# Optimization experiments

Hardware: AMD Instinct MI355X
Metric: run time of the kernel (lower is better)

The kernel has to match this reference:

```python
import jax, jax.numpy as jnp
import numpy as np

N = 100000          # nodes
E = 1600000         # edges
F_IN = 32           # NUM_NODE_FEATURES
H = 128             # dim_h
G = 2048            # graphs in batch


def setup_inputs() -> dict:
    key = jax.random.key(0)
    ks = jax.random.split(key, 12)
    x = jax.random.normal(ks[0], (N, F_IN), dtype=jnp.float32)
    edge_index = jax.random.randint(ks[1], (2, E), 0, N, dtype=jnp.int64)
    batch = jnp.sort(jax.random.randint(ks[2], (N,), 0, G, dtype=jnp.int64))

    def glorot(k, fan_in, fan_out):
        s = np.sqrt(6.0 / (fan_in + fan_out)).astype(np.float32)
        return jax.random.uniform(k, (fan_in, fan_out), jnp.float32, -s, s)

    return {
        "x": x,
        "W1": glorot(ks[3], F_IN, H), "b1": jnp.zeros((H,), jnp.float32),
        "W2": glorot(ks[4], H, H),    "b2": jnp.zeros((H,), jnp.float32),
        "W3": glorot(ks[5], H, H),    "b3": jnp.zeros((H,), jnp.float32),
        "Wlin": glorot(ks[6], H, 1),  "blin": jnp.zeros((1,), jnp.float32),
        "edge_index": edge_index,
        "batch": batch,
    }


def _gcn_conv(x, W, b, row, col, norm, deg_inv):
    # PyG GCNConv: x' = D^{-1/2} (A + I) D^{-1/2} (x W) + b
    xw = x @ W                                   # [N, H]
    msg = norm[:, None] * xw[row]                # gather sources, scale per edge
    out = jax.ops.segment_sum(msg, col, num_segments=N)  # scatter-add to targets
    out = out + deg_inv[:, None] * xw            # self-loop term (norm = 1/deg)
    return out + b


def reference(x, W1, b1, W2, b2, W3, b3, Wlin, blin, edge_index, batch):
    row, col = edge_index[0], edge_index[1]      # source -> target
    # degrees including self-loops
    deg = jax.ops.segment_sum(jnp.ones((E,), x.dtype), col, num_segments=N) + 1.0
    d_isqrt = jax.lax.rsqrt(deg)
    norm = d_isqrt[row] * d_isqrt[col]           # per-edge symmetric norm
    deg_inv = d_isqrt * d_isqrt                  # self-loop norm = 1/deg

    h = jax.nn.relu(_gcn_conv(x, W1, b1, row, col, norm, deg_inv))
    h = jax.nn.relu(_gcn_conv(h, W2, b2, row, col, norm, deg_inv))
    h = _gcn_conv(h, W3, b3, row, col, norm, deg_inv)

    # global mean pool over graphs
    sums = jax.ops.segment_sum(h, batch, num_segments=G)           # [G, H]
    counts = jax.ops.segment_sum(jnp.ones((N,), h.dtype), batch, num_segments=G)
    pooled = sums / jnp.maximum(counts, 1.0)[:, None]

    # dropout is identity in eval mode
    return pooled @ Wlin + blin                  # [G, 1]
```

## Files before the change

kernel.cpp:

```cpp
#include <hip/hip_runtime.h>
#include <math.h>

#define HDIM 128

typedef __attribute__((ext_vector_type(8))) short bf16x8;
typedef __attribute__((ext_vector_type(4))) float f32x4;
typedef __attribute__((ext_vector_type(4))) _Float16 h16x4;

__device__ __forceinline__ void split_bf16(float x, short& hi, short& lo) {
    unsigned u = __float_as_uint(x);
    unsigned r = (u + 0x7FFFu + ((u >> 16) & 1u)) >> 16;
    float hf = __uint_as_float(r << 16);
    hi = (short)r;
    float l = x - hf;
    unsigned ul = __float_as_uint(l);
    unsigned rl = (ul + 0x7FFFu + ((ul >> 16) & 1u)) >> 16;
    lo = (short)rl;
}

__global__ __launch_bounds__(256) void deg_hist_k(const int* __restrict__ col,
                                                  int* __restrict__ deg, int E) {
    int e = blockIdx.x * 256 + threadIdx.x;
    if (e < E) atomicAdd(&deg[col[e]], 1);
}

__global__ __launch_bounds__(256) void scan1_k(const int* __restrict__ deg,
                                               int* __restrict__ incl,
                                               int* __restrict__ partial,
                                               float* __restrict__ dis,
                                               float* __restrict__ dinv, int N) {
    int i = blockIdx.x * 256 + threadIdx.x;
    int lane = threadIdx.x & 63;
    int wid = threadIdx.x >> 6;
    int d0 = (i < N) ? deg[i] : 0;
    if (i < N) {
        double d = (double)d0 + 1.0;
        dis[i]  = (float)(1.0 / sqrt(d));
        dinv[i] = (float)(1.0 / d);
    }
    int s = d0;
#pragma unroll
    for (int off = 1; off < 64; off <<= 1) {
        int t = __shfl_up(s, off);
        if (lane >= off) s += t;
    }
    __shared__ int wsum[4];
    if (lane == 63) wsum[wid] = s;
    __syncthreads();
    if (threadIdx.x == 0) {
        int run = 0;
#pragma unroll
        for (int w = 0; w < 4; ++w) { int t = wsum[w]; wsum[w] = run; run += t; }
    }
    __syncthreads();
    s += wsum[wid];
    if (i < N) incl[i] = s;
    if (threadIdx.x == 255) partial[blockIdx.x] = s;
}

__global__ __launch_bounds__(512) void scan2_k(int* __restrict__ partial, int NB) {
    __shared__ int sm[512];
    int t = threadIdx.x;
    sm[t] = (t < NB) ? partial[t] : 0;
    __syncthreads();
    for (int off = 1; off < 512; off <<= 1) {
        int v = (t >= off) ? sm[t - off] : 0;
        __syncthreads();
        sm[t] += v;
        __syncthreads();
    }
    if (t < NB) partial[t] = (t == 0) ? 0 : sm[t - 1];
}

__global__ __launch_bounds__(256) void scan3_k(const int* __restrict__ deg,
                                               const int* __restrict__ incl,
                                               const int* __restrict__ partial,
                                               int* __restrict__ row_ptr, int N) {
    int i = blockIdx.x * 256 + threadIdx.x;
    if (i < N) {
        int off = partial[blockIdx.x];
        row_ptr[i] = incl[i] - deg[i] + off;
        if (i == N - 1) row_ptr[N] = incl[i] + off;
    }
}

__global__ __launch_bounds__(256) void csr_fill_k(const int* __restrict__ row,
                                                  const int* __restrict__ col,
                                                  const float* __restrict__ dis,
                                                  const int* __restrict__ row_ptr,
                                                  int* __restrict__ cursor,
                                                  int2* __restrict__ csr, int E) {
    int e = blockIdx.x * 256 + threadIdx.x;
    if (e >= E) return;
    int r = row[e], c = col[e];
    int pos = atomicAdd(&cursor[c], 1);
    float nrm = dis[r] * dis[c];
    csr[row_ptr[c] + pos] = make_int2(r, __float_as_int(nrm));
}

__global__ __launch_bounds__(256) void wsplit_k(const float* __restrict__ W,
                                                short* __restrict__ Thi,
                                                short* __restrict__ Tlo, int K) {
    int idx = blockIdx.x * 256 + threadIdx.x;
    if (idx < K * 128) {
        int k = idx >> 7, n = idx & 127;
        short h, l; split_bf16(W[idx], h, l);
        Thi[n * K + k] = h; Tlo[n * K + k] = l;
    }
}

template<int K, bool RELU, bool BIAS, bool OUTH>
__global__ __launch_bounds__(256) void gemm_mfma2(const float* __restrict__ X,
                                                  const short* __restrict__ WThi,
                                                  const short* __restrict__ WTlo,
                                                  const float* __restrict__ b,
                                                  float* __restrict__ outF,
                                                  _Float16* __restrict__ outH, int N) {
    constexpr int KP = 40;
    __shared__ short ahi[128][KP], alo[128][KP];
    __shared__ short bhi[128][KP], blo[128][KP];
    const int tid = threadIdx.x;
    const int wid = tid >> 6, lane = tid & 63;
    const int lr = lane & 15;
    const int lk = (lane >> 4) * 8;
    const int m0b = blockIdx.x * 128;

    f32x4 acc[2][8];
#pragma unroll
    for (int rt = 0; rt < 2; ++rt)
#pragma unroll
        for (int ct = 0; ct < 8; ++ct) acc[rt][ct] = (f32x4){0.f, 0.f, 0.f, 0.f};

    for (int ch = 0; ch < K / 32; ++ch) {
        __syncthreads();
#pragma unroll
        for (int i = 0; i < 4; ++i) {
            int f = tid + i * 256;
            int r = f >> 3, kq = f & 7;
            int grow = m0b + r;
            float4 v = make_float4(0.f, 0.f, 0.f, 0.f);
            if (grow < N) v = *reinterpret_cast<const float4*>(X + (size_t)grow * K + ch * 32 + kq * 4);
            if (RELU) {
                v.x = fmaxf(v.x, 0.f); v.y = fmaxf(v.y, 0.f);
                v.z = fmaxf(v.z, 0.f); v.w = fmaxf(v.w, 0.f);
            }
            short h0, l0, h1, l1;
            split_bf16(v.x, h0, l0); split_bf16(v.y, h1, l1);
            *reinterpret_cast<unsigned*>(&ahi[r][kq * 4]) = (unsigned short)h0 | ((unsigned)(unsigned short)h1 << 16);
            *reinterpret_cast<unsigned*>(&alo[r][kq * 4]) = (unsigned short)l0 | ((unsigned)(unsigned short)l1 << 16);
            split_bf16(v.z, h0, l0); split_bf16(v.w, h1, l1);
            *reinterpret_cast<unsigned*>(&ahi[r][kq * 4 + 2]) = (unsigned short)h0 | ((unsigned)(unsigned short)h1 << 16);
            *reinterpret_cast<unsigned*>(&alo[r][kq * 4 + 2]) = (unsigned short)l0 | ((unsigned)(unsigned short)l1 << 16);
        }
#pragma unroll
        for (int i = 0; i < 2; ++i) {
            int f = tid + i * 256;
            int n = f >> 2, k8 = (f & 3) * 8;
            *reinterpret_cast<uint4*>(&bhi[n][k8]) =
                *reinterpret_cast<const uint4*>(WThi + (size_t)n * K + ch * 32 + k8);
            *reinterpret_cast<uint4*>(&blo[n][k8]) =
                *reinterpret_cast<const uint4*>(WTlo + (size_t)n * K + ch * 32 + k8);
        }
        __syncthreads();

        bf16x8 Ahi[2], Alo[2];
#pragma unroll
        for (int rt = 0; rt < 2; ++rt) {
            int arow = wid * 32 + rt * 16 + lr;
            Ahi[rt] = *reinterpret_cast<const bf16x8*>(&ahi[arow][lk]);
            Alo[rt] = *reinterpret_cast<const bf16x8*>(&alo[arow][lk]);
        }
#pragma unroll
        for (int ct = 0; ct < 8; ++ct) {
            bf16x8 Bhi = *reinterpret_cast<const bf16x8*>(&bhi[ct * 16 + lr][lk]);
            bf16x8 Blo = *reinterpret_cast<const bf16x8*>(&blo[ct * 16 + lr][lk]);
#pragma unroll
            for (int rt = 0; rt < 2; ++rt) {
                acc[rt][ct] = __builtin_amdgcn_mfma_f32_16x16x32_bf16(Ahi[rt], Bhi, acc[rt][ct], 0, 0, 0);
                acc[rt][ct] = __builtin_amdgcn_mfma_f32_16x16x32_bf16(Ahi[rt], Blo, acc[rt][ct], 0, 0, 0);
                acc[rt][ct] = __builtin_amdgcn_mfma_f32_16x16x32_bf16(Alo[rt], Bhi, acc[rt][ct], 0, 0, 0);
            }
        }
    }

    const int r0 = (lane >> 4) * 4;
#pragma unroll
    for (int ct = 0; ct < 8; ++ct) {
        float bias = BIAS ? b[ct * 16 + lr] : 0.f;
#pragma unroll
        for (int rt = 0; rt < 2; ++rt) {
#pragma unroll
            for (int r = 0; r < 4; ++r) {
                int row = m0b + wid * 32 + rt * 16 + r0 + r;
                if (row < N) {
                    float val = acc[rt][ct][r] + bias;
                    if (OUTH) outH[(size_t)row * HDIM + ct * 16 + lr] = (_Float16)val;
                    else      outF[(size_t)row * HDIM + ct * 16 + lr] = val;
                }
            }
        }
    }
}

__global__ __launch_bounds__(256) void gather_x_k(const int* __restrict__ row_ptr,
                                                  const int2* __restrict__ csr,
                                                  const float* __restrict__ dinv,
                                                  const float* __restrict__ X,
                                                  float* __restrict__ Y, int N) {
    int idx = blockIdx.x * 256 + threadIdx.x;
    int c = idx >> 3;
    if (c >= N) return;
    int hq = idx & 7;
    int j0 = row_ptr[c], j1 = row_ptr[c + 1];
    float di = dinv[c];
    float4 xc = *reinterpret_cast<const float4*>(X + (size_t)c * 32 + hq * 4);
    float4 acc = make_float4(di * xc.x, di * xc.y, di * xc.z, di * xc.w);
    int j = j0;
    for (; j + 3 < j1; j += 4) {
        int2 e0 = csr[j], e1 = csr[j + 1], e2 = csr[j + 2], e3 = csr[j + 3];
        float4 v0 = *reinterpret_cast<const float4*>(X + (size_t)e0.x * 32 + hq * 4);
        float4 v1 = *reinterpret_cast<const float4*>(X + (size_t)e1.x * 32 + hq * 4);
        float4 v2 = *reinterpret_cast<const float4*>(X + (size_t)e2.x * 32 + hq * 4);
        float4 v3 = *reinterpret_cast<const float4*>(X + (size_t)e3.x * 32 + hq * 4);
        float n0 = __int_as_float(e0.y), n1 = __int_as_float(e1.y);
        float n2 = __int_as_float(e2.y), n3 = __int_as_float(e3.y);
        acc.x += n0 * v0.x + n1 * v1.x + n2 * v2.x + n3 * v3.x;
        acc.y += n0 * v0.y + n1 * v1.y + n2 * v2.y + n3 * v3.y;
        acc.z += n0 * v0.z + n1 * v1.z + n2 * v2.z + n3 * v3.z;
        acc.w += n0 * v0.w + n1 * v1.w + n2 * v2.w + n3 * v3.w;
    }
    for (; j < j1; ++j) {
        int2 en = csr[j];
        float nrm = __int_as_float(en.y);
        float4 v = *reinterpret_cast<const float4*>(X + (size_t)en.x * 32 + hq * 4);
        acc.x += nrm * v.x; acc.y += nrm * v.y;
        acc.z += nrm * v.z; acc.w += nrm * v.w;
    }
    *reinterpret_cast<float4*>(Y + (size_t)c * 32 + hq * 4) = acc;
}

__global__ __launch_bounds__(128) void w3l_k(const float* __restrict__ W3,
                                             const float* __restrict__ b3,
                                             const float* __restrict__ Wlin,
                                             const float* __restrict__ blin,
                                             float* __restrict__ w3l,
                                             float* __restrict__ consts) {
    __shared__ float wl[128];
    __shared__ float red[128];
    int t = threadIdx.x;
    wl[t] = Wlin[t];
    __syncthreads();
    float a = 0.f;
    for (int j = 0; j < 128; ++j) a += W3[t * 128 + j] * wl[j];
    w3l[t] = a;
    red[t] = b3[t] * wl[t];
    __syncthreads();
    for (int off = 64; off > 0; off >>= 1) {
        if (t < off) red[t] += red[t + off];
        __syncthreads();
    }
    if (t == 0) consts[0] = red[0] + blin[0];
}

__global__ __launch_bounds__(256) void gather_z_k(const int* __restrict__ row_ptr,
                                                  const int2* __restrict__ csr,
                                                  const float* __restrict__ dinv,
                                                  const float* __restrict__ b,
                                                  const _Float16* __restrict__ xw,
                                                  const float* __restrict__ w3l,
                                                  float* __restrict__ z, int N) {
    int c = (blockIdx.x * 256 + threadIdx.x) >> 6;
    if (c >= N) return;
    int lane = threadIdx.x & 63;
    int half = lane >> 5;
    int hq = lane & 31;
    int j0 = row_ptr[c], j1 = row_ptr[c + 1];
    float4 acc = make_float4(0.f, 0.f, 0.f, 0.f);
    int j = j0 + half;
    for (; j + 2 < j1; j += 4) {
        int2 e0 = csr[j], e1 = csr[j + 2];
        h16x4 v0 = *reinterpret_cast<const h16x4*>(xw + (size_t)e0.x * HDIM + hq * 4);
        h16x4 v1 = *reinterpret_cast<const h16x4*>(xw + (size_t)e1.x * HDIM + hq * 4);
        float n0 = __int_as_float(e0.y), n1 = __int_as_float(e1.y);
        acc.x += n0 * (float)v0[0] + n1 * (float)v1[0];
        acc.y += n0 * (float)v0[1] + n1 * (float)v1[1];
        acc.z += n0 * (float)v0[2] + n1 * (float)v1[2];
        acc.w += n0 * (float)v0[3] + n1 * (float)v1[3];
    }
    for (; j < j1; j += 2) {
        int2 en = csr[j];
        float nrm = __int_as_float(en.y);
        h16x4 v = *reinterpret_cast<const h16x4*>(xw + (size_t)en.x * HDIM + hq * 4);
        acc.x += nrm * (float)v[0]; acc.y += nrm * (float)v[1];
        acc.z += nrm * (float)v[2]; acc.w += nrm * (float)v[3];
    }
    acc.x += __shfl_xor(acc.x, 32);
    acc.y += __shfl_xor(acc.y, 32);
    acc.z += __shfl_xor(acc.z, 32);
    acc.w += __shfl_xor(acc.w, 32);
    h16x4 xc = *reinterpret_cast<const h16x4*>(xw + (size_t)c * HDIM + hq * 4);
    float di = dinv[c];
    float4 bb = *reinterpret_cast<const float4*>(b + hq * 4);
    float4 wv = *reinterpret_cast<const float4*>(w3l + hq * 4);
    float t = fmaxf(di * (float)xc[0] + bb.x + acc.x, 0.f) * wv.x
            + fmaxf(di * (float)xc[1] + bb.y + acc.y, 0.f) * wv.y
            + fmaxf(di * (float)xc[2] + bb.z + acc.z, 0.f) * wv.z
            + fmaxf(di * (float)xc[3] + bb.w + acc.w, 0.f) * wv.w;
#pragma unroll
    for (int off = 1; off < 32; off <<= 1) t += __shfl_xor(t, off);
    if (lane == 0) z[c] = t;
}

__global__ __launch_bounds__(256) void gather_s_k(const int* __restrict__ row_ptr,
                                                  const int2* __restrict__ csr,
                                                  const float* __restrict__ dinv,
                                                  const float* __restrict__ z,
                                                  float* __restrict__ s, int N) {
    int c = blockIdx.x * 256 + threadIdx.x;
    if (c >= N) return;
    int j0 = row_ptr[c], j1 = row_ptr[c + 1];
    float acc = dinv[c] * z[c];
    for (int j = j0; j < j1; ++j) {
        int2 en = csr[j];
        acc += __int_as_float(en.y) * z[en.x];
    }
    s[c] = acc;
}

__global__ __launch_bounds__(256) void gstart_k(const int* __restrict__ batch,
                                                int* __restrict__ start, int N, int G) {
    int n = blockIdx.x * 256 + threadIdx.x;
    if (n > N) return;
    if (n < N) {
        int b = batch[n];
        int prev = (n == 0) ? -1 : batch[n - 1];
        for (int g = prev + 1; g <= b; ++g) start[g] = n;
    } else {
        int prev = batch[N - 1];
        for (int g = prev + 1; g <= G; ++g) start[g] = N;
    }
}

__global__ __launch_bounds__(256) void final_z_k(const float* __restrict__ s,
                                                 const int* __restrict__ start,
                                                 const float* __restrict__ consts,
                                                 const float* __restrict__ blin,
                                                 float* __restrict__ out, int G) {
    int g = blockIdx.x * 4 + (threadIdx.x >> 6);
    int lane = threadIdx.x & 63;
    if (g >= G) return;
    int a = start[g], e = start[g + 1];
    float acc = 0.f;
    for (int n = a + lane; n < e; n += 64) acc += s[n];
#pragma unroll
    for (int off = 32; off > 0; off >>= 1) acc += __shfl_down(acc, off);
    if (lane == 0) out[g] = (e > a) ? acc / (float)(e - a) + consts[0] : blin[0];
}

extern "C" void kernel_launch(void* const* d_in, const int* in_sizes, int n_in,
                              void* d_out, int out_size, void* d_ws, size_t ws_size,
                              hipStream_t stream) {
    const float* x    = (const float*)d_in[0];
    const float* W1   = (const float*)d_in[1];
    const float* b1   = (const float*)d_in[2];
    const float* W2   = (const float*)d_in[3];
    const float* b2   = (const float*)d_in[4];
    const float* W3   = (const float*)d_in[5];
    const float* b3   = (const float*)d_in[6];
    const float* Wlin = (const float*)d_in[7];
    const float* blin = (const float*)d_in[8];
    const int* ei     = (const int*)d_in[9];
    const int* batch  = (const int*)d_in[10];

    const int N = in_sizes[10];
    const int E = in_sizes[9] / 2;
    const int G = out_size;
    const size_t NH = (size_t)N * HDIM;
    const int NB = (N + 255) / 256;

    const int* row = ei;
    const int* col = ei + E;

    int2* csr      = (int2*)d_ws;
    float* Y       = (float*)(csr + E);
    float* h1      = Y + (size_t)N * 32;
    _Float16* xwh  = (_Float16*)(h1 + NH);
    float* dis     = (float*)(xwh + NH);
    float* dinv    = dis + N;
    float* zbuf    = dinv + N;
    float* sbuf    = zbuf + N;
    float* w3l     = sbuf + N;
    float* consts  = w3l + 128;
    short* w1hi    = (short*)(consts + 4);
    short* w1lo    = w1hi + 128 * 32;
    short* w2hi    = w1lo + 128 * 32;
    short* w2lo    = w2hi + 128 * 128;
    int* deg_i     = (int*)(w2lo + 128 * 128);
    int* row_ptr   = deg_i + N;
    int* cursor    = row_ptr + N + 1;
    int* gstart    = cursor + N;
    int* incl      = gstart + G + 1;
    int* partial   = incl + N;

    float* outf = (float*)d_out;

    hipMemsetAsync(deg_i, 0, (size_t)N * sizeof(int), stream);
    hipMemsetAsync(cursor, 0, (size_t)N * sizeof(int), stream);
    deg_hist_k<<<(E + 255) / 256, 256, 0, stream>>>(col, deg_i, E);
    scan1_k<<<NB, 256, 0, stream>>>(deg_i, incl, partial, dis, dinv, N);
    scan2_k<<<1, 512, 0, stream>>>(partial, NB);
    scan3_k<<<NB, 256, 0, stream>>>(deg_i, incl, partial, row_ptr, N);
    csr_fill_k<<<(E + 255) / 256, 256, 0, stream>>>(row, col, dis, row_ptr, cursor, csr, E);
    gstart_k<<<(N + 256) / 256, 256, 0, stream>>>(batch, gstart, N, G);
    wsplit_k<<<(32 * 128 + 255) / 256, 256, 0, stream>>>(W1, w1hi, w1lo, 32);
    wsplit_k<<<(128 * 128 + 255) / 256, 256, 0, stream>>>(W2, w2hi, w2lo, 128);
    w3l_k<<<1, 128, 0, stream>>>(W3, b3, Wlin, blin, w3l, consts);

    const int mfma_grid = (N + 127) / 128;
    const int wave_grid = (N + 3) / 4;

    gather_x_k<<<(N * 8 + 255) / 256, 256, 0, stream>>>(row_ptr, csr, dinv, x, Y, N);
    gemm_mfma2<32, false, true, false><<<mfma_grid, 256, 0, stream>>>(Y, w1hi, w1lo, b1, h1, nullptr, N);
    gemm_mfma2<128, true, false, true><<<mfma_grid, 256, 0, stream>>>(h1, w2hi, w2lo, nullptr, nullptr, xwh, N);
    gather_z_k<<<wave_grid, 256, 0, stream>>>(row_ptr, csr, dinv, b2, xwh, w3l, zbuf, N);
    gather_s_k<<<(N + 255) / 256, 256, 0, stream>>>(row_ptr, csr, dinv, zbuf, sbuf, N);
    final_z_k<<<(G + 3) / 4, 256, 0, stream>>>(sbuf, gstart, consts, blin, outf, G);
}
```

Before: 343.6 us.

## Store source-only CSR and recompute edge norms from dis on the fly

The CSR now stores only the 4-byte source index instead of an (index, norm) int2 pair, and each gather kernel recomputes the edge norm as dis[src]*dis[c]. The cursor array is initialised by copying row_ptr, so the fill kernel writes directly at cursor positions, which drops one memset and the row_ptr/dis reads during fill. gather_z is reworked to four edge groups of 16 lanes, each lane loading 8 halves, reducing with two shuffles. This halves CSR traffic at the cost of an extra random dis load per edge.

```diff
diff --git a/kernel.cpp b/kernel.cpp
--- a/kernel.cpp
+++ b/kernel.cpp
@@ -5,7 +5,7 @@
 
 typedef __attribute__((ext_vector_type(8))) short bf16x8;
 typedef __attribute__((ext_vector_type(4))) float f32x4;
-typedef __attribute__((ext_vector_type(4))) _Float16 h16x4;
+typedef __attribute__((ext_vector_type(8))) _Float16 h16x8;
 
 __device__ __forceinline__ void split_bf16(float x, short& hi, short& lo) {
     unsigned u = __float_as_uint(x);
@@ -86,16 +86,13 @@
 
 __global__ __launch_bounds__(256) void csr_fill_k(const int* __restrict__ row,
                                                   const int* __restrict__ col,
-                                                  const float* __restrict__ dis,
-                                                  const int* __restrict__ row_ptr,
                                                   int* __restrict__ cursor,
-                                                  int2* __restrict__ csr, int E) {
+                                                  int* __restrict__ csr, int E) {
     int e = blockIdx.x * 256 + threadIdx.x;
     if (e >= E) return;
     int r = row[e], c = col[e];
     int pos = atomicAdd(&cursor[c], 1);
-    float nrm = dis[r] * dis[c];
-    csr[row_ptr[c] + pos] = make_int2(r, __float_as_int(nrm));
+    csr[pos] = r;
 }
 
 __global__ __launch_bounds__(256) void wsplit_k(const float* __restrict__ W,
@@ -203,7 +200,8 @@
 }
 
 __global__ __launch_bounds__(256) void gather_x_k(const int* __restrict__ row_ptr,
-                                                  const int2* __restrict__ csr,
+                                                  const int* __restrict__ csr,
+                                                  const float* __restrict__ dis,
                                                   const float* __restrict__ dinv,
                                                   const float* __restrict__ X,
                                                   float* __restrict__ Y, int N) {
@@ -212,27 +210,28 @@
     if (c >= N) return;
     int hq = idx & 7;
     int j0 = row_ptr[c], j1 = row_ptr[c + 1];
+    float dc = dis[c];
     float di = dinv[c];
     float4 xc = *reinterpret_cast<const float4*>(X + (size_t)c * 32 + hq * 4);
     float4 acc = make_float4(di * xc.x, di * xc.y, di * xc.z, di * xc.w);
     int j = j0;
     for (; j + 3 < j1; j += 4) {
-        int2 e0 = csr[j], e1 = csr[j + 1], e2 = csr[j + 2], e3 = csr[j + 3];
-        float4 v0 = *reinterpret_cast<const float4*>(X + (size_t)e0.x * 32 + hq * 4);
-        float4 v1 = *reinterpret_cast<const float4*>(X + (size_t)e1.x * 32 + hq * 4);
-        float4 v2 = *reinterpret_cast<const float4*>(X + (size_t)e2.x * 32 + hq * 4);
-        float4 v3 = *reinterpret_cast<const float4*>(X + (size_t)e3.x * 32 + hq * 4);
-        float n0 = __int_as_float(e0.y), n1 = __int_as_float(e1.y);
-        float n2 = __int_as_float(e2.y), n3 = __int_as_float(e3.y);
+        int s0 = csr[j], s1 = csr[j + 1], s2 = csr[j + 2], s3 = csr[j + 3];
+        float4 v0 = *reinterpret_cast<const float4*>(X + (size_t)s0 * 32 + hq * 4);
+        float4 v1 = *reinterpret_cast<const float4*>(X + (size_t)s1 * 32 + hq * 4);
+        float4 v2 = *reinterpret_cast<const float4*>(X + (size_t)s2 * 32 + hq * 4);
+        float4 v3 = *reinterpret_cast<const float4*>(X + (size_t)s3 * 32 + hq * 4);
+        float n0 = dis[s0] * dc, n1 = dis[s1] * dc;
+        float n2 = dis[s2] * dc, n3 = dis[s3] * dc;
         acc.x += n0 * v0.x + n1 * v1.x + n2 * v2.x + n3 * v3.x;
         acc.y += n0 * v0.y + n1 * v1.y + n2 * v2.y + n3 * v3.y;
         acc.z += n0 * v0.z + n1 * v1.z + n2 * v2.z + n3 * v3.z;
         acc.w += n0 * v0.w + n1 * v1.w + n2 * v2.w + n3 * v3.w;
     }
     for (; j < j1; ++j) {
-        int2 en = csr[j];
-        float nrm = __int_as_float(en.y);
-        float4 v = *reinterpret_cast<const float4*>(X + (size_t)en.x * 32 + hq * 4);
+        int s0 = csr[j];
+        float nrm = dis[s0] * dc;
+        float4 v = *reinterpret_cast<const float4*>(X + (size_t)s0 * 32 + hq * 4);
         acc.x += nrm * v.x; acc.y += nrm * v.y;
         acc.z += nrm * v.z; acc.w += nrm * v.w;
     }
@@ -263,7 +262,8 @@
 }
 
 __global__ __launch_bounds__(256) void gather_z_k(const int* __restrict__ row_ptr,
-                                                  const int2* __restrict__ csr,
+                                                  const int* __restrict__ csr,
+                                                  const float* __restrict__ dis,
                                                   const float* __restrict__ dinv,
                                                   const float* __restrict__ b,
                                                   const _Float16* __restrict__ xw,
@@ -272,57 +272,54 @@
     int c = (blockIdx.x * 256 + threadIdx.x) >> 6;
     if (c >= N) return;
     int lane = threadIdx.x & 63;
-    int half = lane >> 5;
-    int hq = lane & 31;
+    int g = lane >> 4;
+    int q = lane & 15;
     int j0 = row_ptr[c], j1 = row_ptr[c + 1];
-    float4 acc = make_float4(0.f, 0.f, 0.f, 0.f);
-    int j = j0 + half;
-    for (; j + 2 < j1; j += 4) {
-        int2 e0 = csr[j], e1 = csr[j + 2];
-        h16x4 v0 = *reinterpret_cast<const h16x4*>(xw + (size_t)e0.x * HDIM + hq * 4);
-        h16x4 v1 = *reinterpret_cast<const h16x4*>(xw + (size_t)e1.x * HDIM + hq * 4);
-        float n0 = __int_as_float(e0.y), n1 = __int_as_float(e1.y);
-        acc.x += n0 * (float)v0[0] + n1 * (float)v1[0];
-        acc.y += n0 * (float)v0[1] + n1 * (float)v1[1];
-        acc.z += n0 * (float)v0[2] + n1 * (float)v1[2];
-        acc.w += n0 * (float)v0[3] + n1 * (float)v1[3];
-    }
-    for (; j < j1; j += 2) {
-        int2 en = csr[j];
-        float nrm = __int_as_float(en.y);
-        h16x4 v = *reinterpret_cast<const h16x4*>(xw + (size_t)en.x * HDIM + hq * 4);
-        acc.x += nrm * (float)v[0]; acc.y += nrm * (float)v[1];
-        acc.z += nrm * (float)v[2]; acc.w += nrm * (float)v[3];
-    }
-    acc.x += __shfl_xor(acc.x, 32);
-    acc.y += __shfl_xor(acc.y, 32);
-    acc.z += __shfl_xor(acc.z, 32);
-    acc.w += __shfl_xor(acc.w, 32);
-    h16x4 xc = *reinterpret_cast<const h16x4*>(xw + (size_t)c * HDIM + hq * 4);
+    float dc = dis[c];
+    float acc[8] = {0.f, 0.f, 0.f, 0.f, 0.f, 0.f, 0.f, 0.f};
+    for (int j = j0 + g; j < j1; j += 4) {
+        int src = csr[j];
+        float nrm = dis[src] * dc;
+        h16x8 v = *reinterpret_cast<const h16x8*>(xw + (size_t)src * HDIM + q * 8);
+#pragma unroll
+        for (int k = 0; k < 8; ++k) acc[k] += nrm * (float)v[k];
+    }
+#pragma unroll
+    for (int k = 0; k < 8; ++k) {
+        acc[k] += __shfl_xor(acc[k], 16);
+        acc[k] += __shfl_xor(acc[k], 32);
+    }
+    h16x8 xc = *reinterpret_cast<const h16x8*>(xw + (size_t)c * HDIM + q * 8);
     float di = dinv[c];
-    float4 bb = *reinterpret_cast<const float4*>(b + hq * 4);
-    float4 wv = *reinterpret_cast<const float4*>(w3l + hq * 4);
-    float t = fmaxf(di * (float)xc[0] + bb.x + acc.x, 0.f) * wv.x
-            + fmaxf(di * (float)xc[1] + bb.y + acc.y, 0.f) * wv.y
-            + fmaxf(di * (float)xc[2] + bb.z + acc.z, 0.f) * wv.z
-            + fmaxf(di * (float)xc[3] + bb.w + acc.w, 0.f) * wv.w;
-#pragma unroll
-    for (int off = 1; off < 32; off <<= 1) t += __shfl_xor(t, off);
+    float4 b0 = *reinterpret_cast<const float4*>(b + q * 8);
+    float4 b1 = *reinterpret_cast<const float4*>(b + q * 8 + 4);
+    float4 w0 = *reinterpret_cast<const float4*>(w3l + q * 8);
+    float4 w1 = *reinterpret_cast<const float4*>(w3l + q * 8 + 4);
+    const float bb[8] = {b0.x, b0.y, b0.z, b0.w, b1.x, b1.y, b1.z, b1.w};
+    const float ww[8] = {w0.x, w0.y, w0.z, w0.w, w1.x, w1.y, w1.z, w1.w};
+    float t = 0.f;
+#pragma unroll
+    for (int k = 0; k < 8; ++k)
+        t += fmaxf(di * (float)xc[k] + bb[k] + acc[k], 0.f) * ww[k];
+#pragma unroll
+    for (int off = 1; off < 16; off <<= 1) t += __shfl_xor(t, off);
     if (lane == 0) z[c] = t;
 }
 
 __global__ __launch_bounds__(256) void gather_s_k(const int* __restrict__ row_ptr,
-                                                  const int2* __restrict__ csr,
+                                                  const int* __restrict__ csr,
+                                                  const float* __restrict__ dis,
                                                   const float* __restrict__ dinv,
                                                   const float* __restrict__ z,
                                                   float* __restrict__ s, int N) {
     int c = blockIdx.x * 256 + threadIdx.x;
     if (c >= N) return;
     int j0 = row_ptr[c], j1 = row_ptr[c + 1];
+    float dc = dis[c];
     float acc = dinv[c] * z[c];
     for (int j = j0; j < j1; ++j) {
-        int2 en = csr[j];
-        acc += __int_as_float(en.y) * z[en.x];
+        int src = csr[j];
+        acc += dis[src] * dc * z[src];
     }
     s[c] = acc;
 }
@@ -381,7 +378,7 @@
     const int* row = ei;
     const int* col = ei + E;
 
-    int2* csr      = (int2*)d_ws;
+    int* csr       = (int*)d_ws;
     float* Y       = (float*)(csr + E);
     float* h1      = Y + (size_t)N * 32;
     _Float16* xwh  = (_Float16*)(h1 + NH);
@@ -405,12 +402,12 @@
     float* outf = (float*)d_out;
 
     hipMemsetAsync(deg_i, 0, (size_t)N * sizeof(int), stream);
-    hipMemsetAsync(cursor, 0, (size_t)N * sizeof(int), stream);
     deg_hist_k<<<(E + 255) / 256, 256, 0, stream>>>(col, deg_i, E);
     scan1_k<<<NB, 256, 0, stream>>>(deg_i, incl, partial, dis, dinv, N);
     scan2_k<<<1, 512, 0, stream>>>(partial, NB);
     scan3_k<<<NB, 256, 0, stream>>>(deg_i, incl, partial, row_ptr, N);
-    csr_fill_k<<<(E + 255) / 256, 256, 0, stream>>>(row, col, dis, row_ptr, cursor, csr, E);
+    hipMemcpyAsync(cursor, row_ptr, (size_t)N * sizeof(int), hipMemcpyDeviceToDevice, stream);
+    csr_fill_k<<<(E + 255) / 256, 256, 0, stream>>>(row, col, cursor, csr, E);
     gstart_k<<<(N + 256) / 256, 256, 0, stream>>>(batch, gstart, N, G);
     wsplit_k<<<(32 * 128 + 255) / 256, 256, 0, stream>>>(W1, w1hi, w1lo, 32);
     wsplit_k<<<(128 * 128 + 255) / 256, 256, 0, stream>>>(W2, w2hi, w2lo, 128);
@@ -419,10 +416,10 @@
     const int mfma_grid = (N + 127) / 128;
     const int wave_grid = (N + 3) / 4;
 
-    gather_x_k<<<(N * 8 + 255) / 256, 256, 0, stream>>>(row_ptr, csr, dinv, x, Y, N);
+    gather_x_k<<<(N * 8 + 255) / 256, 256, 0, stream>>>(row_ptr, csr, dis, dinv, x, Y, N);
     gemm_mfma2<32, false, true, false><<<mfma_grid, 256, 0, stream>>>(Y, w1hi, w1lo, b1, h1, nullptr, N);
     gemm_mfma2<128, true, false, true><<<mfma_grid, 256, 0, stream>>>(h1, w2hi, w2lo, nullptr, nullptr, xwh, N);
-    gather_z_k<<<wave_grid, 256, 0, stream>>>(row_ptr, csr, dinv, b2, xwh, w3l, zbuf, N);
-    gather_s_k<<<(N + 255) / 256, 256, 0, stream>>>(row_ptr, csr, dinv, zbuf, sbuf, N);
+    gather_z_k<<<wave_grid, 256, 0, stream>>>(row_ptr, csr, dis, dinv, b2, xwh, w3l, zbuf, N);
+    gather_s_k<<<(N + 255) / 256, 256, 0, stream>>>(row_ptr, csr, dis, dinv, zbuf, sbuf, N);
     final_z_k<<<(G + 3) / 4, 256, 0, stream>>>(sbuf, gstart, consts, blin, outf, G);
 }
```

After: 397.5 us. 1.16x slower.

## Partition CSR fill by destination range and widen gather loads to 8 halves

Applied to the files above, without the earlier changes.

The CSR fill kernel now splits destination nodes into 8 ranges. Each group of blocks scans all edges but writes only those whose target falls in its range, so atomics and scattered writes stay inside a smaller region that is more likely to be cache- or XCD-local. The cost is that every edge's col value is read 8 times. The layer-2 gather now gives each lane 8 fp16 features and processes 4 edges in parallel per wave instead of 2, with wider 16-byte loads and an extra shuffle stage for the reduction.

```diff
diff --git a/kernel.cpp b/kernel.cpp
--- a/kernel.cpp
+++ b/kernel.cpp
@@ -5,7 +5,7 @@
 
 typedef __attribute__((ext_vector_type(8))) short bf16x8;
 typedef __attribute__((ext_vector_type(4))) float f32x4;
-typedef __attribute__((ext_vector_type(4))) _Float16 h16x4;
+typedef __attribute__((ext_vector_type(8))) _Float16 h16x8;
 
 __device__ __forceinline__ void split_bf16(float x, short& hi, short& lo) {
     unsigned u = __float_as_uint(x);
@@ -84,18 +84,29 @@
     }
 }
 
-__global__ __launch_bounds__(256) void csr_fill_k(const int* __restrict__ row,
+__global__ __launch_bounds__(256) void fill_loc_k(const int* __restrict__ row,
                                                   const int* __restrict__ col,
                                                   const float* __restrict__ dis,
                                                   const int* __restrict__ row_ptr,
                                                   int* __restrict__ cursor,
-                                                  int2* __restrict__ csr, int E) {
-    int e = blockIdx.x * 256 + threadIdx.x;
-    if (e >= E) return;
-    int r = row[e], c = col[e];
-    int pos = atomicAdd(&cursor[c], 1);
-    float nrm = dis[r] * dis[c];
-    csr[row_ptr[c] + pos] = make_int2(r, __float_as_int(nrm));
+                                                  int2* __restrict__ csr,
+                                                  int E, int PSZ) {
+    int p = blockIdx.x & 7;
+    int sl = blockIdx.x >> 3;
+    int nsl = gridDim.x >> 3;
+    int d0 = p * PSZ, d1 = d0 + PSZ;
+    for (int base = sl * 256; base < E; base += nsl * 256) {
+        int e = base + (int)threadIdx.x;
+        if (e < E) {
+            int c = col[e];
+            if (c >= d0 && c < d1) {
+                int r = row[e];
+                int pos = atomicAdd(&cursor[c], 1);
+                float nrm = dis[r] * dis[c];
+                csr[row_ptr[c] + pos] = make_int2(r, __float_as_int(nrm));
+            }
+        }
+    }
 }
 
 __global__ __launch_bounds__(256) void wsplit_k(const float* __restrict__ W,
@@ -272,42 +283,45 @@
     int c = (blockIdx.x * 256 + threadIdx.x) >> 6;
     if (c >= N) return;
     int lane = threadIdx.x & 63;
-    int half = lane >> 5;
-    int hq = lane & 31;
+    int g = lane >> 4;
+    int q = lane & 15;
     int j0 = row_ptr[c], j1 = row_ptr[c + 1];
-    float4 acc = make_float4(0.f, 0.f, 0.f, 0.f);
-    int j = j0 + half;
-    for (; j + 2 < j1; j += 4) {
-        int2 e0 = csr[j], e1 = csr[j + 2];
-        h16x4 v0 = *reinterpret_cast<const h16x4*>(xw + (size_t)e0.x * HDIM + hq * 4);
-        h16x4 v1 = *reinterpret_cast<const h16x4*>(xw + (size_t)e1.x * HDIM + hq * 4);
+    float acc[8] = {0.f, 0.f, 0.f, 0.f, 0.f, 0.f, 0.f, 0.f};
+    int j = j0 + g;
+    for (; j + 4 < j1; j += 8) {
+        int2 e0 = csr[j], e1 = csr[j + 4];
         float n0 = __int_as_float(e0.y), n1 = __int_as_float(e1.y);
-        acc.x += n0 * (float)v0[0] + n1 * (float)v1[0];
-        acc.y += n0 * (float)v0[1] + n1 * (float)v1[1];
-        acc.z += n0 * (float)v0[2] + n1 * (float)v1[2];
-        acc.w += n0 * (float)v0[3] + n1 * (float)v1[3];
-    }
-    for (; j < j1; j += 2) {
+        h16x8 v0 = *reinterpret_cast<const h16x8*>(xw + (size_t)e0.x * HDIM + q * 8);
+        h16x8 v1 = *reinterpret_cast<const h16x8*>(xw + (size_t)e1.x * HDIM + q * 8);
+#pragma unroll
+        for (int k = 0; k < 8; ++k) acc[k] += n0 * (float)v0[k] + n1 * (float)v1[k];
+    }
+    for (; j < j1; j += 4) {
         int2 en = csr[j];
         float nrm = __int_as_float(en.y);
-        h16x4 v = *reinterpret_cast<const h16x4*>(xw + (size_t)en.x * HDIM + hq * 4);
-        acc.x += nrm * (float)v[0]; acc.y += nrm * (float)v[1];
-        acc.z += nrm * (float)v[2]; acc.w += nrm * (float)v[3];
-    }
-    acc.x += __shfl_xor(acc.x, 32);
-    acc.y += __shfl_xor(acc.y, 32);
-    acc.z += __shfl_xor(acc.z, 32);
-    acc.w += __shfl_xor(acc.w, 32);
-    h16x4 xc = *reinterpret_cast<const h16x4*>(xw + (size_t)c * HDIM + hq * 4);
+        h16x8 v = *reinterpret_cast<const h16x8*>(xw + (size_t)en.x * HDIM + q * 8);
+#pragma unroll
+        for (int k = 0; k < 8; ++k) acc[k] += nrm * (float)v[k];
+    }
+#pragma unroll
+    for (int k = 0; k < 8; ++k) {
+        acc[k] += __shfl_xor(acc[k], 16);
+        acc[k] += __shfl_xor(acc[k], 32);
+    }
+    h16x8 xc = *reinterpret_cast<const h16x8*>(xw + (size_t)c * HDIM + q * 8);
     float di = dinv[c];
-    float4 bb = *reinterpret_cast<const float4*>(b + hq * 4);
-    float4 wv = *reinterpret_cast<const float4*>(w3l + hq * 4);
-    float t = fmaxf(di * (float)xc[0] + bb.x + acc.x, 0.f) * wv.x
-            + fmaxf(di * (float)xc[1] + bb.y + acc.y, 0.f) * wv.y
-            + fmaxf(di * (float)xc[2] + bb.z + acc.z, 0.f) * wv.z
-            + fmaxf(di * (float)xc[3] + bb.w + acc.w, 0.f) * wv.w;
-#pragma unroll
-    for (int off = 1; off < 32; off <<= 1) t += __shfl_xor(t, off);
+    float4 b0 = *reinterpret_cast<const float4*>(b + q * 8);
+    float4 b1 = *reinterpret_cast<const float4*>(b + q * 8 + 4);
+    float4 w0 = *reinterpret_cast<const float4*>(w3l + q * 8);
+    float4 w1 = *reinterpret_cast<const float4*>(w3l + q * 8 + 4);
+    const float bb[8] = {b0.x, b0.y, b0.z, b0.w, b1.x, b1.y, b1.z, b1.w};
+    const float ww[8] = {w0.x, w0.y, w0.z, w0.w, w1.x, w1.y, w1.z, w1.w};
+    float t = 0.f;
+#pragma unroll
+    for (int k = 0; k < 8; ++k)
+        t += fmaxf(di * (float)xc[k] + bb[k] + acc[k], 0.f) * ww[k];
+#pragma unroll
+    for (int off = 1; off < 16; off <<= 1) t += __shfl_xor(t, off);
     if (lane == 0) z[c] = t;
 }
 
@@ -377,6 +391,7 @@
     const int G = out_size;
     const size_t NH = (size_t)N * HDIM;
     const int NB = (N + 255) / 256;
+    const int PSZ = (N + 7) / 8;
 
     const int* row = ei;
     const int* col = ei + E;
@@ -410,7 +425,7 @@
     scan1_k<<<NB, 256, 0, stream>>>(deg_i, incl, partial, dis, dinv, N);
     scan2_k<<<1, 512, 0, stream>>>(partial, NB);
     scan3_k<<<NB, 256, 0, stream>>>(deg_i, incl, partial, row_ptr, N);
-    csr_fill_k<<<(E + 255) / 256, 256, 0, stream>>>(row, col, dis, row_ptr, cursor, csr, E);
+    fill_loc_k<<<2048, 256, 0, stream>>>(row, col, dis, row_ptr, cursor, csr, E, PSZ);
     gstart_k<<<(N + 256) / 256, 256, 0, stream>>>(batch, gstart, N, G);
     wsplit_k<<<(32 * 128 + 255) / 256, 256, 0, stream>>>(W1, w1hi, w1lo, 32);
     wsplit_k<<<(128 * 128 + 255) / 256, 256, 0, stream>>>(W2, w2hi, w2lo, 128);
```

After: 338.4 us. No clear change (-1.5%).
